# Kernel optimization log

Measured on AMD Instinct MI355X. Metric: run time of the kernel, lower is better.

The kernel has to match this reference:

```python
import jax, jax.numpy as jnp
import numpy as np

NUM_RBF = 16
TOP_K = 30
MAX_REL = 32
EDGE_FEATURES = 128
EDGE_IN = 16 + NUM_RBF * 16  # pos emb + 16 RBF blocks


def _rbf(D):
    # D [..., ] -> [..., NUM_RBF]
    D_mu = jnp.linspace(2.0, 22.0, NUM_RBF)
    D_sigma = (22.0 - 2.0) / NUM_RBF
    return jnp.exp(-(((D[..., None] - D_mu) / D_sigma) ** 2))


def _pair_dist(A, B):
    # A,B [B,L,3] -> [B,L,L] dist from each i (rows) to each j (cols)
    return jnp.sqrt(jnp.sum((A[:, :, None, :] - B[:, None, :, :]) ** 2, -1) + 1e-6)


def _gather_rbf(A, B, E_idx):
    D = _pair_dist(A, B)                      # [B,L,L]
    Dn = jnp.take_along_axis(D, E_idx, axis=2)  # [B,L,K]
    return _rbf(Dn)                           # [B,L,K,NUM_RBF]


def setup_inputs() -> dict:
    key = jax.random.key(0)
    ks = jax.random.split(key, 6)
    Bb, L = 4, 2048
    X = jax.random.normal(ks[0], (Bb, L, 4, 3), dtype=jnp.float32) * 3.0
    mask = jnp.ones((Bb, L), dtype=jnp.float32)
    residue_idx = jnp.broadcast_to(jnp.arange(L, dtype=jnp.int64), (Bb, L))
    chain_labels = jax.random.randint(ks[1], (Bb, L), 0, 2).astype(jnp.int64)
    pe_w = jax.random.normal(ks[2], (16, 2 * MAX_REL + 2), dtype=jnp.float32) * 0.1
    pe_b = jnp.zeros((16,), dtype=jnp.float32)
    edge_w = jax.random.normal(ks[3], (EDGE_FEATURES, EDGE_IN), dtype=jnp.float32) * 0.05
    ln_g = jnp.ones((EDGE_FEATURES,), dtype=jnp.float32)
    ln_b = jnp.zeros((EDGE_FEATURES,), dtype=jnp.float32)
    return {"X": X, "mask": mask, "residue_idx": residue_idx,
            "chain_labels": chain_labels, "pe_w": pe_w, "pe_b": pe_b,
            "edge_w": edge_w, "ln_g": ln_g, "ln_b": ln_b}


def reference(X, mask, residue_idx, chain_labels, pe_w, pe_b, edge_w, ln_g, ln_b):
    # virtual Cb construction
    b = X[:, :, 2, :] - X[:, :, 0, :]
    c = X[:, :, 1, :] - X[:, :, 2, :]
    a = jnp.cross(b, c)
    Cb = -0.58273431 * a + 0.56802827 * b - 0.54067466 * c + X[:, :, 2, :]
    N = X[:, :, 0, :]
    C = X[:, :, 1, :]
    Ca = X[:, :, 2, :]

    # kNN graph on C coordinates (masked distances)
    mask2d = mask[:, None, :] * mask[:, :, None]          # [B,L,L]
    dX = C[:, None, :, :] - C[:, :, None, :]
    D = mask2d * jnp.sqrt(jnp.sum(dX ** 2, -1) + 1e-6)
    D_max = jnp.max(D, -1, keepdims=True)
    D_adjust = D + (1.0 - mask2d) * D_max
    k = min(TOP_K, X.shape[1])
    neg_vals, E_idx = jax.lax.top_k(-D_adjust, k)          # smallest k, ascending
    D_neighbors = -neg_vals                                # [B,L,K]

    # 16 RBF blocks
    pairs = [(N, N), (Ca, Ca), (Cb, Cb), (C, N), (C, Ca), (C, Cb),
             (N, Ca), (N, Cb), (Cb, Ca), (N, C), (Ca, C), (Cb, C),
             (Ca, N), (Cb, N), (Ca, Cb)]
    RBF_all = [_rbf(D_neighbors)] + [_gather_rbf(A, B2, E_idx) for (A, B2) in pairs]
    RBF_all = jnp.concatenate(RBF_all, axis=-1)            # [B,L,K,256]

    # positional encodings
    offset = residue_idx[:, :, None] - residue_idx[:, None, :]
    offset = jnp.take_along_axis(offset, E_idx, axis=2)    # [B,L,K]
    d_chains = (chain_labels[:, :, None] - chain_labels[:, None, :] == 0).astype(jnp.int32)
    E_chains = jnp.take_along_axis(d_chains, E_idx, axis=2)
    d = jnp.clip(offset + MAX_REL, 0, 2 * MAX_REL) * E_chains + (1 - E_chains) * (2 * MAX_REL + 1)
    d_onehot = jax.nn.one_hot(d, 2 * MAX_REL + 2, dtype=jnp.float32)
    E_positional = jnp.einsum('blkc,nc->blkn', d_onehot, pe_w) + pe_b

    # edge embedding + layernorm
    E = jnp.concatenate((E_positional, RBF_all), axis=-1)  # [B,L,K,272]
    E = jnp.einsum('blkc,fc->blkf', E, edge_w)
    mu = jnp.mean(E, -1, keepdims=True)
    var = jnp.mean((E - mu) ** 2, -1, keepdims=True)
    E = (E - mu) / jnp.sqrt(var + 1e-5) * ln_g + ln_b
    return (E, E_idx)
```

## Files before the change

### kernel.cpp

```cpp
#include <hip/hip_runtime.h>
#include <cfloat>
#include <cstdint>

#define B_DIM 4
#define L_DIM 2048
#define NROW (B_DIM * L_DIM)
#define TOPK 30
#define NEDGE (NROW * TOPK)

#define WS_CB    0
#define WS_CX    24576
#define WS_CY    32768
#define WS_CZ    40960
#define WS_TPOS  49152
#define WS_BPACK 57600
#define WS_EIDX  73984

typedef __bf16 bf16x8 __attribute__((ext_vector_type(8)));
typedef __bf16 bf16x2 __attribute__((ext_vector_type(2)));
typedef float f32x4 __attribute__((ext_vector_type(4)));

static __device__ __forceinline__ unsigned short f2bf(float x) {
  unsigned u = __float_as_uint(x);
  unsigned r = (u + 0x7fffu + ((u >> 16) & 1u)) >> 16;
  return (unsigned short)r;
}

static __device__ __forceinline__ unsigned pk_bf16(float a, float b) {
#if __has_builtin(__builtin_amdgcn_cvt_pk_bf16_f32)
  union { bf16x2 v; unsigned u; } cv;
  cv.v = __builtin_amdgcn_cvt_pk_bf16_f32(a, b);
  return cv.u;
#else
  return (unsigned)f2bf(a) | ((unsigned)f2bf(b) << 16);
#endif
}

static __device__ __forceinline__ unsigned wave_min_u32_dpp(unsigned v) {
#if __has_builtin(__builtin_amdgcn_update_dpp) && __has_builtin(__builtin_amdgcn_readlane)
  int x = (int)v, t;
  t = __builtin_amdgcn_update_dpp(x, x, 0x111, 0xf, 0xf, false);
  x = ((unsigned)t < (unsigned)x) ? t : x;
  t = __builtin_amdgcn_update_dpp(x, x, 0x112, 0xf, 0xf, false);
  x = ((unsigned)t < (unsigned)x) ? t : x;
  t = __builtin_amdgcn_update_dpp(x, x, 0x114, 0xf, 0xf, false);
  x = ((unsigned)t < (unsigned)x) ? t : x;
  t = __builtin_amdgcn_update_dpp(x, x, 0x118, 0xf, 0xf, false);
  x = ((unsigned)t < (unsigned)x) ? t : x;
  t = __builtin_amdgcn_update_dpp(x, x, 0x142, 0xa, 0xf, false);
  x = ((unsigned)t < (unsigned)x) ? t : x;
  t = __builtin_amdgcn_update_dpp(x, x, 0x143, 0xc, 0xf, false);
  x = ((unsigned)t < (unsigned)x) ? t : x;
  return (unsigned)__builtin_amdgcn_readlane(x, 63);
#else
  unsigned mv = v;
  #pragma unroll
  for (int off = 32; off; off >>= 1) {
    unsigned o = __shfl_xor(mv, off);
    mv = o < mv ? o : mv;
  }
  return mv;
#endif
}

__global__ void prep_kernel(const float* __restrict__ X,
                            const float* __restrict__ pe_w,
                            const float* __restrict__ pe_b,
                            const float* __restrict__ edge_w,
                            float* __restrict__ ws) {
  int tid = blockIdx.x * 256 + threadIdx.x;
  if (tid < NROW) {
    const float* Xr = X + (size_t)tid * 12;
    float nx = Xr[0], ny = Xr[1], nz = Xr[2];
    float cx = Xr[3], cy = Xr[4], cz = Xr[5];
    float ax = Xr[6], ay = Xr[7], az = Xr[8];
    float bx = ax - nx, by = ay - ny, bz = az - nz;
    float vx = cx - ax, vy = cy - ay, vz = cz - az;
    float crx = by * vz - bz * vy;
    float cry = bz * vx - bx * vz;
    float crz = bx * vy - by * vx;
    ws[WS_CB + tid * 3 + 0] = -0.58273431f * crx + 0.56802827f * bx - 0.54067466f * vx + ax;
    ws[WS_CB + tid * 3 + 1] = -0.58273431f * cry + 0.56802827f * by - 0.54067466f * vy + ay;
    ws[WS_CB + tid * 3 + 2] = -0.58273431f * crz + 0.56802827f * bz - 0.54067466f * vz + az;
    ws[WS_CX + tid] = cx;
    ws[WS_CY + tid] = cy;
    ws[WS_CZ + tid] = cz;
  } else if (tid < NROW + 8448) {
    int t2 = tid - NROW;
    int d = t2 >> 7, f = t2 & 127;
    float s = 0.f;
    #pragma unroll
    for (int n = 0; n < 16; n++)
      s += edge_w[f * 272 + n] * (pe_w[n * 66 + d] + pe_b[n]);
    ws[WS_TPOS + t2] = s;
  } else if (tid < NROW + 8448 + 16384) {
    int i2 = tid - NROW - 8448;
    int j2 = i2 & 3;
    int lane = (i2 >> 2) & 63;
    int s = (i2 >> 8) & 1;
    int nt = (i2 >> 9) & 7;
    int c = (i2 >> 12) & 3;
    int f = nt * 16 + (lane & 15);
    int k = c * 64 + s * 32 + (lane >> 4) * 8 + j2 * 2;
    float v0 = edge_w[f * 272 + 16 + k];
    float v1 = edge_w[f * 272 + 16 + k + 1];
    unsigned out = (unsigned)f2bf(v0) | ((unsigned)f2bf(v1) << 16);
    ((unsigned*)(ws + WS_BPACK))[i2] = out;
  }
}

#define CAS64(a, b) { bool lt = (a) < (b); \
  unsigned long long lo = lt ? (a) : (b), hi = lt ? (b) : (a); (a) = lo; (b) = hi; }

__global__ void __launch_bounds__(256)
topk_kernel(const float* __restrict__ ws,
            const float* __restrict__ mask,
            int* __restrict__ eidx_out,
            float* __restrict__ idxf_out) {
  int row = blockIdx.x;
  int b = row >> 11;
  int li = row & 2047;
  int t = threadIdx.x;
  int lane = t & 63;
  int w = t >> 6;

  __shared__ float s_red[4];
  __shared__ unsigned long long s_cand[128];
  __shared__ unsigned long long s_q[4 * 6 * 64];

  const float* Cx = ws + WS_CX + b * L_DIM;
  const float* Cy = ws + WS_CY + b * L_DIM;
  const float* Cz = ws + WS_CZ + b * L_DIM;

  float cix = Cx[li], ciy = Cy[li], ciz = Cz[li];
  float mi = mask[row];

  float dloc[8], m2l[8];
  float dmax = 0.f;
  #pragma unroll
  for (int i = 0; i < 8; i++) {
    int j = w * 512 + i * 64 + lane;
    float dx = Cx[j] - cix;
    float dy = Cy[j] - ciy;
    float dz = Cz[j] - ciz;
    float raw = sqrtf(dx * dx + dy * dy + dz * dz + 1e-6f);
    float m2 = mi * mask[b * L_DIM + j];
    float d = m2 * raw;
    dloc[i] = d;
    m2l[i] = m2;
    dmax = fmaxf(dmax, d);
  }
  #pragma unroll
  for (int off = 32; off; off >>= 1)
    dmax = fmaxf(dmax, __shfl_xor(dmax, off));
  if (lane == 0) s_red[w] = dmax;
  __syncthreads();
  dmax = fmaxf(fmaxf(s_red[0], s_red[1]), fmaxf(s_red[2], s_red[3]));

  unsigned long long key[8];
  #pragma unroll
  for (int i = 0; i < 8; i++) {
    float v = dloc[i] + (1.f - m2l[i]) * dmax;
    int j = w * 512 + i * 64 + lane;
    key[i] = ((unsigned long long)__float_as_uint(v) << 32) | (unsigned)j;
  }
  CAS64(key[0], key[1]); CAS64(key[2], key[3]); CAS64(key[4], key[5]); CAS64(key[6], key[7]);
  CAS64(key[0], key[2]); CAS64(key[1], key[3]); CAS64(key[4], key[6]); CAS64(key[5], key[7]);
  CAS64(key[1], key[2]); CAS64(key[5], key[6]); CAS64(key[0], key[4]); CAS64(key[3], key[7]);
  CAS64(key[1], key[5]); CAS64(key[2], key[6]);
  CAS64(key[1], key[4]); CAS64(key[3], key[6]);
  CAS64(key[2], key[4]); CAS64(key[3], key[5]);
  CAS64(key[3], key[4]);

  #pragma unroll
  for (int s = 2; s < 8; s++)
    s_q[(w * 6 + (s - 2)) * 64 + lane] = key[s];

  unsigned cv = (unsigned)(key[0] >> 32);
  unsigned cj = (unsigned)key[0];
  unsigned long long nxt = key[1];
  int ptr = 0;

  unsigned long long myout = ~0ull;

  for (int n = 0; n < TOPK; n++) {
    unsigned mv = wave_min_u32_dpp(cv);
    unsigned long long ball = __ballot(cv == mv);
    if (ball == 0) ball = 1;
    unsigned wj;
    bool me;
    if (__popcll(ball) == 1) {
      int wl = (int)__builtin_ctzll(ball);
#if __has_builtin(__builtin_amdgcn_readlane)
      wj = (unsigned)__builtin_amdgcn_readlane((int)cj, wl);
#else
      wj = (unsigned)__shfl((int)cj, wl);
#endif
      me = (lane == wl);
    } else {
      unsigned tj = (cv == mv) ? cj : 0xffffffffu;
      unsigned mj = tj;
      #pragma unroll
      for (int off = 32; off; off >>= 1) {
        unsigned o = __shfl_xor(mj, off);
        mj = o < mj ? o : mj;
      }
      wj = mj;
      me = (cv == mv) && (cj == mj);
    }
    if (lane == n)
      myout = ((unsigned long long)mv << 32) | wj;
    if (me) {
      cv = (unsigned)(nxt >> 32);
      cj = (unsigned)nxt;
      nxt = (ptr < 6) ? s_q[(w * 6 + ptr) * 64 + lane] : ~0ull;
      ptr++;
    }
  }
  if (lane < 32)
    s_cand[w * 32 + lane] = (lane < TOPK) ? myout : ~0ull;
  __syncthreads();

  if (w == 0) {
    unsigned long long c0 = s_cand[lane];
    unsigned long long c1 = s_cand[64 + lane];
    bool lowhalf = lane < 32;

    #define MERGE32(c) { \
      unsigned long long p = __shfl_xor((c), 63); \
      (c) = (c) < p ? (c) : p; \
      _Pragma("unroll") \
      for (int j = 16; j; j >>= 1) { \
        unsigned long long q = __shfl_xor((c), j); \
        bool up = (lane & j) == 0; \
        unsigned long long mn = (c) < q ? (c) : q; \
        unsigned long long mx = (c) < q ? q : (c); \
        (c) = up ? mn : mx; \
      } }

    MERGE32(c0); MERGE32(c1);
    c0 = lowhalf ? c0 : c1;
    MERGE32(c0);
    #undef MERGE32

    if (lane < TOPK) {
      int j = (int)(c0 & 0xffffffffull);
      eidx_out[row * TOPK + lane] = j;
      idxf_out[row * TOPK + lane] = (float)j;
    }
  }
}

#define PA_BITS 0x2323203001113201ull
#define PB_BITS 0x3001112323203201ull

#define SM_DIST 0
#define SM_A    4352
#define SM_B    12544
#define SM_POS  28928
#define SM_TOTAL 29184

__global__ void __launch_bounds__(256)
edge_kernel(const float* __restrict__ X,
            const float* __restrict__ ws,
            const int* __restrict__ ridx,
            const int* __restrict__ chain,
            const float* __restrict__ ln_g,
            const float* __restrict__ ln_b,
            float* __restrict__ out) {
  __shared__ __align__(16) char smem[SM_TOTAL];
  float* s_dist = (float*)(smem + SM_DIST);
  int* s_pos = (int*)(smem + SM_POS);

  int t = threadIdx.x;
  int r0 = blockIdx.x * 2;
  const float* Cbw = ws + WS_CB;
  const float* Tpos = ws + WS_TPOS;
  const int* eidx = (const int*)(ws + WS_EIDX);

  if (t < 240) {
    int e = t >> 2, q = t & 3;
    int row = r0 + (e >= 30 ? 1 : 0);
    int kn = e - (e >= 30 ? 30 : 0);
    int bb = row >> 11;
    int j = eidx[row * TOPK + kn];
    int jrow = bb * L_DIM + j;
    if (q == 0) {
      int off = ridx[row] - ridx[jrow];
      int same = (chain[row] == chain[jrow]);
      s_pos[e] = same ? min(max(off + 32, 0), 64) : 65;
    }
    const float4* Xi4 = (const float4*)(X + (size_t)row * 12);
    const float4* Xj4 = (const float4*)(X + (size_t)jrow * 12);
    float4 i0 = Xi4[0], i1 = Xi4[1];
    float4 j0 = Xj4[0], j1 = Xj4[1];
    float i2x = X[(size_t)row * 12 + 8];
    float j2x = X[(size_t)jrow * 12 + 8];
    float axi[4], ayi[4], azi[4], axj[4], ayj[4], azj[4];
    axi[0] = i0.x; ayi[0] = i0.y; azi[0] = i0.z;
    axi[1] = i0.w; ayi[1] = i1.x; azi[1] = i1.y;
    axi[2] = i1.z; ayi[2] = i1.w; azi[2] = i2x;
    axi[3] = Cbw[row * 3 + 0]; ayi[3] = Cbw[row * 3 + 1]; azi[3] = Cbw[row * 3 + 2];
    axj[0] = j0.x; ayj[0] = j0.y; azj[0] = j0.z;
    axj[1] = j0.w; ayj[1] = j1.x; azj[1] = j1.y;
    axj[2] = j1.z; ayj[2] = j1.w; azj[2] = j2x;
    axj[3] = Cbw[jrow * 3 + 0]; ayj[3] = Cbw[jrow * 3 + 1]; azj[3] = Cbw[jrow * 3 + 2];
    #pragma unroll
    for (int u = 0; u < 4; u++) {
      int p = q * 4 + u;
      int a = (int)((PA_BITS >> (p * 4)) & 7);
      int bc = (int)((PB_BITS >> (p * 4)) & 7);
      float dx = axi[a] - axj[bc];
      float dy = ayi[a] - ayj[bc];
      float dz = azi[a] - azj[bc];
      s_dist[e * 17 + p] = sqrtf(dx * dx + dy * dy + dz * dz + 1e-6f);
    }
  } else {
    int t2 = t - 240;
    int e = 60 + (t2 >> 2), q = t2 & 3;
    if (q == 0) s_pos[e] = 0;
    #pragma unroll
    for (int u = 0; u < 4; u++) s_dist[e * 17 + q * 4 + u] = 8.0f;
  }
  __syncthreads();

  int lane = t & 63;
  int w = t >> 6;

  f32x4 zero4 = {0.f, 0.f, 0.f, 0.f};
  f32x4 acc[8];
  #pragma unroll
  for (int nt = 0; nt < 8; nt++) acc[nt] = zero4;

  const float C1 = 0.96089792702916f;
  const float DC = 1.28119723603888f;
  const float B0 = -1.92179585405832f;

  for (int c = 0; c < 4; c++) {
    {
      const float4* src = (const float4*)(ws + WS_BPACK) + c * 1024;
      float4* dst = (float4*)(smem + SM_B);
      #pragma unroll
      for (int v = 0; v < 4; v++) dst[t + v * 256] = src[t + v * 256];
    }
    {
      unsigned* ap = (unsigned*)(smem + SM_A);
      #pragma unroll
      for (int v = 0; v < 8; v++) {
        int i2 = t + v * 256;
        int j2 = i2 & 3;
        int al = (i2 >> 2) & 63;
        int s = (i2 >> 8) & 1;
        int aw = (i2 >> 9) & 3;
        int m = aw * 16 + (al & 15);
        int k = c * 64 + s * 32 + (al >> 4) * 8 + j2 * 2;
        float d = s_dist[m * 17 + (k >> 4)];
        float rrf = (float)(k & 15);
        float base = fmaf(rrf, -DC, B0);
        float zs0 = fmaf(d, C1, base);
        float zs1 = zs0 - DC;
        float v0 = __builtin_exp2f(-zs0 * zs0);
        float v1 = __builtin_exp2f(-zs1 * zs1);
        ap[i2] = pk_bf16(v0, v1);
      }
    }
    __syncthreads();
    #pragma unroll
    for (int s = 0; s < 2; s++) {
      bf16x8 a = *(const bf16x8*)(smem + SM_A + ((w * 2 + s) * 64 + lane) * 16);
      #pragma unroll
      for (int nt = 0; nt < 8; nt++) {
        bf16x8 bfr = *(const bf16x8*)(smem + SM_B + ((nt * 2 + s) * 64 + lane) * 16);
        acc[nt] = __builtin_amdgcn_mfma_f32_16x16x32_bf16(a, bfr, acc[nt], 0, 0, 0);
      }
    }
    __syncthreads();
  }

  int quad = lane >> 4;
  int col0 = lane & 15;
  #pragma unroll
  for (int r = 0; r < 4; r++) {
    int e = w * 16 + quad * 4 + r;
    bool live = (e < 60);
    int dp = live ? s_pos[e] : 0;
    const float* tp = Tpos + dp * 128;
    float vv[8];
    float s = 0.f, s2 = 0.f;
    #pragma unroll
    for (int nt = 0; nt < 8; nt++) {
      float x = acc[nt][r] + tp[nt * 16 + col0];
      vv[nt] = x;
      s += x;
      s2 += x * x;
    }
    #pragma unroll
    for (int off = 8; off; off >>= 1) {
      s += __shfl_xor(s, off, 16);
      s2 += __shfl_xor(s2, off, 16);
    }
    float mu = s * (1.0f / 128.0f);
    float var = s2 * (1.0f / 128.0f) - mu * mu;
    float inv = rsqrtf(var + 1e-5f);
    if (live) {
      int row = r0 + (e >= 30 ? 1 : 0);
      int kn = e - (e >= 30 ? 30 : 0);
      float* o = out + ((size_t)row * TOPK + kn) * 128;
      #pragma unroll
      for (int nt = 0; nt < 8; nt++) {
        int f = nt * 16 + col0;
        o[f] = (vv[nt] - mu) * inv * ln_g[f] + ln_b[f];
      }
    }
  }
}

extern "C" void kernel_launch(void* const* d_in, const int* in_sizes, int n_in,
                              void* d_out, int out_size, void* d_ws, size_t ws_size,
                              hipStream_t stream) {
  const float* X      = (const float*)d_in[0];
  const float* mask   = (const float*)d_in[1];
  const int*   ridx   = (const int*)d_in[2];
  const int*   chain  = (const int*)d_in[3];
  const float* pe_w   = (const float*)d_in[4];
  const float* pe_b   = (const float*)d_in[5];
  const float* edge_w = (const float*)d_in[6];
  const float* ln_g   = (const float*)d_in[7];
  const float* ln_b   = (const float*)d_in[8];
  float* out = (float*)d_out;
  float* ws  = (float*)d_ws;

  hipLaunchKernelGGL(prep_kernel, dim3(129), dim3(256), 0, stream,
                     X, pe_w, pe_b, edge_w, ws);
  hipLaunchKernelGGL(topk_kernel, dim3(NROW), dim3(256), 0, stream,
                     ws, mask, (int*)(ws + WS_EIDX), out + (size_t)NEDGE * 128);
  hipLaunchKernelGGL(edge_kernel, dim3(NROW / 2), dim3(256), 0, stream,
                     X, ws, ridx, chain, ln_g, ln_b, out);
}
```

Measured before the change: 248.6 us.

## Double-buffer B tiles and build A fragments directly in registers

The kernel now builds the RBF A-operand fragments straight into registers instead of writing them to shared memory and reading them back. The B-weight staging into shared memory is double-buffered so the next chunk loads while the current chunk's MFMAs run, which cuts the barriers per chunk from two to one. The barrier after the distance computation is dropped. That is safe only because each wavefront reads just the distance rows it wrote itself. The cost is more shared memory for the second B buffer and more register pressure from the held fragments.

```diff
diff --git a/kernel.cpp b/kernel.cpp
--- a/kernel.cpp
+++ b/kernel.cpp
@@ -255,10 +255,9 @@
 #define PB_BITS 0x3001112323203201ull
 
 #define SM_DIST 0
-#define SM_A    4352
-#define SM_B    12544
-#define SM_POS  28928
-#define SM_TOTAL 29184
+#define SM_POS  4352
+#define SM_B    4608
+#define SM_TOTAL 37376
 
 __global__ void __launch_bounds__(256)
 edge_kernel(const float* __restrict__ X,
@@ -322,7 +321,6 @@
     #pragma unroll
     for (int u = 0; u < 4; u++) s_dist[e * 17 + q * 4 + u] = 8.0f;
   }
-  __syncthreads();
 
   int lane = t & 63;
   int w = t >> 6;
@@ -336,46 +334,54 @@
   const float DC = 1.28119723603888f;
   const float B0 = -1.92179585405832f;
 
+  #define STAGE(cc) { \
+    const float4* src = (const float4*)(ws + WS_BPACK) + (cc) * 1024; \
+    float4* dst = (float4*)(smem + SM_B + ((cc) & 1) * 16384); \
+    _Pragma("unroll") \
+    for (int v2 = 0; v2 < 4; v2++) dst[t + v2 * 256] = src[t + v2 * 256]; }
+
+  #define MAKE_AFRAG(dstv, cc, ss) { \
+    union { unsigned u[4]; bf16x8 v; } cvt; \
+    _Pragma("unroll") \
+    for (int j2 = 0; j2 < 4; j2++) { \
+      int k = (cc) * 64 + (ss) * 32 + (lane >> 4) * 8 + j2 * 2; \
+      float d = s_dist[(w * 16 + (lane & 15)) * 17 + (k >> 4)]; \
+      float rrf = (float)(k & 15); \
+      float base = fmaf(rrf, -DC, B0); \
+      float zs0 = fmaf(d, C1, base); \
+      float zs1 = zs0 - DC; \
+      cvt.u[j2] = pk_bf16(__builtin_exp2f(-zs0 * zs0), \
+                          __builtin_exp2f(-zs1 * zs1)); \
+    } \
+    (dstv) = cvt.v; }
+
+  bf16x8 af0, af1;
+  STAGE(0);
+  MAKE_AFRAG(af0, 0, 0);
+  MAKE_AFRAG(af1, 0, 1);
+  __syncthreads();
+
+  #pragma unroll
   for (int c = 0; c < 4; c++) {
-    {
-      const float4* src = (const float4*)(ws + WS_BPACK) + c * 1024;
-      float4* dst = (float4*)(smem + SM_B);
-      #pragma unroll
-      for (int v = 0; v < 4; v++) dst[t + v * 256] = src[t + v * 256];
-    }
-    {
-      unsigned* ap = (unsigned*)(smem + SM_A);
-      #pragma unroll
-      for (int v = 0; v < 8; v++) {
-        int i2 = t + v * 256;
-        int j2 = i2 & 3;
-        int al = (i2 >> 2) & 63;
-        int s = (i2 >> 8) & 1;
-        int aw = (i2 >> 9) & 3;
-        int m = aw * 16 + (al & 15);
-        int k = c * 64 + s * 32 + (al >> 4) * 8 + j2 * 2;
-        float d = s_dist[m * 17 + (k >> 4)];
-        float rrf = (float)(k & 15);
-        float base = fmaf(rrf, -DC, B0);
-        float zs0 = fmaf(d, C1, base);
-        float zs1 = zs0 - DC;
-        float v0 = __builtin_exp2f(-zs0 * zs0);
-        float v1 = __builtin_exp2f(-zs1 * zs1);
-        ap[i2] = pk_bf16(v0, v1);
-      }
-    }
-    __syncthreads();
+    if (c < 3) STAGE(c + 1);
     #pragma unroll
     for (int s = 0; s < 2; s++) {
-      bf16x8 a = *(const bf16x8*)(smem + SM_A + ((w * 2 + s) * 64 + lane) * 16);
+      bf16x8 a = (s == 0) ? af0 : af1;
       #pragma unroll
       for (int nt = 0; nt < 8; nt++) {
-        bf16x8 bfr = *(const bf16x8*)(smem + SM_B + ((nt * 2 + s) * 64 + lane) * 16);
+        bf16x8 bfr = *(const bf16x8*)(smem + SM_B + (c & 1) * 16384 +
+                                      ((nt * 2 + s) * 64 + lane) * 16);
         acc[nt] = __builtin_amdgcn_mfma_f32_16x16x32_bf16(a, bfr, acc[nt], 0, 0, 0);
       }
     }
-    __syncthreads();
-  }
+    if (c < 3) {
+      MAKE_AFRAG(af0, c + 1, 0);
+      MAKE_AFRAG(af1, c + 1, 1);
+      __syncthreads();
+    }
+  }
+  #undef STAGE
+  #undef MAKE_AFRAG
 
   int quad = lane >> 4;
   int col0 = lane & 15;
```

Measured after the change: 240.0 us. 1.04x faster.
